# Kernel tuning notes

Measured on AMD Instinct MI355X. Metric: run time of the kernel, lower is better.

Reference implementation:

```python
import jax, jax.numpy as jnp
import numpy as np

WINDOW_SIZE = 11
CHANNEL = 1
SIGMA = 1.5


def _gaussian_window(window_size=WINDOW_SIZE, channel=CHANNEL, sigma=SIGMA):
    x = np.arange(window_size)
    g = np.exp(-((x - window_size // 2) ** 2) / (2.0 * sigma ** 2))
    g = g / g.sum()
    w2d = np.outer(g, g).astype(np.float32)  # [K,K]
    # depthwise conv kernel: [C_out=channel, C_in/groups=1, K, K]
    return jnp.asarray(np.broadcast_to(w2d, (channel, 1, window_size, window_size)))


def _dwconv(x, window):
    pad = WINDOW_SIZE // 2
    return jax.lax.conv_general_dilated(
        x, window,
        window_strides=(1, 1),
        padding=[(pad, pad), (pad, pad)],
        dimension_numbers=('NCHW', 'OIHW', 'NCHW'),
        feature_group_count=CHANNEL)


def _ssim(img1, img2, window):
    C1 = 0.01 ** 2
    C2 = 0.03 ** 2
    mu1 = _dwconv(img1, window)
    mu2 = _dwconv(img2, window)
    mu1_sq = mu1 * mu1
    mu2_sq = mu2 * mu2
    mu1_mu2 = mu1 * mu2
    sigma1_sq = _dwconv(img1 * img1, window) - mu1_sq
    sigma2_sq = _dwconv(img2 * img2, window) - mu2_sq
    sigma12 = _dwconv(img1 * img2, window) - mu1_mu2
    ssim_map = ((2.0 * mu1_mu2 + C1) * (2.0 * sigma12 + C2)) / (
        (mu1_sq + mu2_sq + C1) * (sigma1_sq + sigma2_sq + C2))
    return ssim_map.mean()


def setup_inputs() -> dict:
    key = jax.random.key(0)
    k1, k2 = jax.random.split(key)
    B, C, H, W = 64, 1, 512, 512
    pred = jax.random.uniform(k1, (B, C, H, W), dtype=jnp.float32)
    target = jax.random.uniform(k2, (B, C, H, W), dtype=jnp.float32)
    return {"pred": pred, "target": target}


def reference(pred, target):
    window = _gaussian_window()
    return 1.0 - _ssim(pred[:, :1], target[:, :1], window)
```

## Files before the change

kernel.cpp:

```cpp
#include <hip/hip_runtime.h>

#define BATCH 64
#define HH 512
#define WW 512
#define TH 32
#define KS 11
#define PADK 5
#define NPIX (64.0 * 512.0 * 512.0)
#define LROW (WW + 2 * PADK)

__global__ void __launch_bounds__(WW) ssim_main_kernel(
    const float* __restrict__ img1, const float* __restrict__ img2,
    double* __restrict__ accum) {
  constexpr float G[KS] = {
      0.00102838f, 0.00759884f, 0.03600087f, 0.10936069f, 0.21300553f,
      0.26601172f, 0.21300553f, 0.10936069f, 0.03600087f, 0.00759884f,
      0.00102838f};

  const int c  = threadIdx.x;
  const int r0 = blockIdx.x * TH;
  const int b  = blockIdx.y;

  const float* __restrict__ p1 = img1 + (size_t)b * (HH * WW);
  const float* __restrict__ p2 = img2 + (size_t)b * (HH * WW);

  __shared__ float2 sh[2][LROW];
  if (c < PADK) {
#pragma unroll
    for (int bi = 0; bi < 2; ++bi) {
      sh[bi][c] = make_float2(0.f, 0.f);
      sh[bi][WW + PADK + c] = make_float2(0.f, 0.f);
    }
  }

  float r1[KS], r2[KS], r11[KS], r22[KS], r12[KS];
#pragma unroll
  for (int k = 0; k < KS; ++k) { r1[k]=0.f; r2[k]=0.f; r11[k]=0.f; r22[k]=0.f; r12[k]=0.f; }

  float local = 0.f;

  float pa = 0.f, pb = 0.f;
  {
    const int rr = r0 - PADK;
    if (rr >= 0) {
      const int off = rr * WW + c;
      pa = p1[off];
      pb = p2[off];
    }
  }

  for (int ii = 0; ii < 4; ++ii) {
#pragma unroll
    for (int p = 0; p < KS; ++p) {
      const int i = ii * KS + p;
      const int buf = i & 1;

      const float ca = pa, cb = pb;
      {
        const int rn = r0 - PADK + i + 1;
        pa = 0.f; pb = 0.f;
        if (rn >= 0 && rn < HH) {
          const int off = rn * WW + c;
          pa = p1[off];
          pb = p2[off];
        }
      }

      sh[buf][PADK + c] = make_float2(ca, cb);
      __syncthreads();

      float h1 = 0.f, h2 = 0.f, h11 = 0.f, h22 = 0.f, h12 = 0.f;
#pragma unroll
      for (int k = 0; k < KS; ++k) {
        const float2 v = sh[buf][c + k];
        const float w  = G[k];
        const float aw = v.x * w;
        const float bw = v.y * w;
        h1  += aw;
        h2  += bw;
        h11 = fmaf(aw, v.x, h11);
        h22 = fmaf(bw, v.y, h22);
        h12 = fmaf(aw, v.y, h12);
      }

      r1[p] = h1; r2[p] = h2; r11[p] = h11; r22[p] = h22; r12[p] = h12;

      if (i >= 2 * PADK && i < TH + 2 * PADK) {
        float mu1 = 0.f, mu2 = 0.f, m11 = 0.f, m22 = 0.f, m12 = 0.f;
#pragma unroll
        for (int t = 0; t < KS; ++t) {
          const int s = (p + 1 + t) % KS;
          const float w = G[t];
          mu1 = fmaf(w, r1[s], mu1);
          mu2 = fmaf(w, r2[s], mu2);
          m11 = fmaf(w, r11[s], m11);
          m22 = fmaf(w, r22[s], m22);
          m12 = fmaf(w, r12[s], m12);
        }
        const float mu1s = mu1 * mu1;
        const float mu2s = mu2 * mu2;
        const float mu12 = mu1 * mu2;
        const float s11 = m11 - mu1s;
        const float s22 = m22 - mu2s;
        const float s12 = m12 - mu12;
        const float C1 = 1e-4f, C2 = 9e-4f;
        const float num = fmaf(2.f, mu12, C1) * fmaf(2.f, s12, C2);
        const float den = (mu1s + mu2s + C1) * (s11 + s22 + C2);
        local = fmaf(num, __builtin_amdgcn_rcpf(den), local);
      }
    }
  }

#pragma unroll
  for (int off = 32; off > 0; off >>= 1) local += __shfl_down(local, off, 64);

  __shared__ float wsum[WW / 64];
  const int wave = threadIdx.x >> 6;
  const int lane = threadIdx.x & 63;
  if (lane == 0) wsum[wave] = local;
  __syncthreads();
  if (threadIdx.x == 0) {
    float s = 0.f;
#pragma unroll
    for (int w = 0; w < WW / 64; ++w) s += wsum[w];
    atomicAdd(accum, (double)s);
  }
}

__global__ void ssim_final_kernel(const double* __restrict__ accum,
                                  float* __restrict__ out) {
  out[0] = 1.0f - (float)(accum[0] / NPIX);
}

extern "C" void kernel_launch(void* const* d_in, const int* in_sizes, int n_in,
                              void* d_out, int out_size, void* d_ws, size_t ws_size,
                              hipStream_t stream) {
  const float* img1 = (const float*)d_in[0];
  const float* img2 = (const float*)d_in[1];
  double* accum = (double*)d_ws;
  hipMemsetAsync(accum, 0, sizeof(double), stream);

  dim3 grid(HH / TH, BATCH);
  ssim_main_kernel<<<grid, WW, 0, stream>>>(img1, img2, accum);
  ssim_final_kernel<<<1, 1, 0, stream>>>(accum, (float*)d_out);
}
```

Measured before the change: 191.7 us.

## Precompute squared terms per pixel, merge sigma sums, batch four rows per sync

Each pixel now stores a float4 (a, b, a²+b², ab) in shared memory, so the horizontal pass runs four FMA chains instead of five and the vertical pass sums sigma1+sigma2 as a single field. Rows are staged four at a time, so there is one barrier per four rows instead of one per row. The outer loop is fully unrolled and launch bounds now request 4 blocks per SM. The trade-off is a larger shared-memory footprint and more register pressure, and the merged sum-of-squares term may lose a little floating-point accuracy.

```diff
diff --git a/kernel.cpp b/kernel.cpp
--- a/kernel.cpp
+++ b/kernel.cpp
@@ -6,10 +6,12 @@
 #define TH 32
 #define KS 11
 #define PADK 5
+#define RCH 4
+#define NCH 11
 #define NPIX (64.0 * 512.0 * 512.0)
 #define LROW (WW + 2 * PADK)
 
-__global__ void __launch_bounds__(WW) ssim_main_kernel(
+__global__ void __launch_bounds__(WW, 4) ssim_main_kernel(
     const float* __restrict__ img1, const float* __restrict__ img2,
     double* __restrict__ accum) {
   constexpr float G[KS] = {
@@ -24,88 +26,92 @@
   const float* __restrict__ p1 = img1 + (size_t)b * (HH * WW);
   const float* __restrict__ p2 = img2 + (size_t)b * (HH * WW);
 
-  __shared__ float2 sh[2][LROW];
+  __shared__ float4 s4[2][RCH][LROW];
   if (c < PADK) {
 #pragma unroll
-    for (int bi = 0; bi < 2; ++bi) {
-      sh[bi][c] = make_float2(0.f, 0.f);
-      sh[bi][WW + PADK + c] = make_float2(0.f, 0.f);
+    for (int bi = 0; bi < 2; ++bi)
+#pragma unroll
+      for (int r = 0; r < RCH; ++r) {
+        s4[bi][r][c]             = make_float4(0.f, 0.f, 0.f, 0.f);
+        s4[bi][r][WW + PADK + c] = make_float4(0.f, 0.f, 0.f, 0.f);
+      }
+  }
+
+  float rA[KS], rB[KS], rQ[KS], rP[KS];
+  float local = 0.f;
+
+  float pa[RCH], pb[RCH];
+#pragma unroll
+  for (int r = 0; r < RCH; ++r) {
+    const int rr = r0 - PADK + r;
+    pa[r] = 0.f; pb[r] = 0.f;
+    if (rr >= 0 && rr < HH) {
+      const int off = rr * WW + c;
+      pa[r] = p1[off];
+      pb[r] = p2[off];
     }
   }
 
-  float r1[KS], r2[KS], r11[KS], r22[KS], r12[KS];
 #pragma unroll
-  for (int k = 0; k < KS; ++k) { r1[k]=0.f; r2[k]=0.f; r11[k]=0.f; r22[k]=0.f; r12[k]=0.f; }
+  for (int ii = 0; ii < NCH; ++ii) {
+    const int buf = ii & 1;
 
-  float local = 0.f;
+#pragma unroll
+    for (int r = 0; r < RCH; ++r) {
+      const float a = pa[r], bb = pb[r];
+      s4[buf][r][PADK + c] = make_float4(a, bb, fmaf(a, a, bb * bb), a * bb);
+    }
+    __syncthreads();
 
-  float pa = 0.f, pb = 0.f;
-  {
-    const int rr = r0 - PADK;
-    if (rr >= 0) {
-      const int off = rr * WW + c;
-      pa = p1[off];
-      pb = p2[off];
-    }
-  }
-
-  for (int ii = 0; ii < 4; ++ii) {
+    if (ii + 1 < NCH) {
 #pragma unroll
-    for (int p = 0; p < KS; ++p) {
-      const int i = ii * KS + p;
-      const int buf = i & 1;
-
-      const float ca = pa, cb = pb;
-      {
-        const int rn = r0 - PADK + i + 1;
-        pa = 0.f; pb = 0.f;
-        if (rn >= 0 && rn < HH) {
-          const int off = rn * WW + c;
-          pa = p1[off];
-          pb = p2[off];
+      for (int r = 0; r < RCH; ++r) {
+        const int rr = r0 - PADK + (ii + 1) * RCH + r;
+        pa[r] = 0.f; pb[r] = 0.f;
+        if (rr >= 0 && rr < HH) {
+          const int off = rr * WW + c;
+          pa[r] = p1[off];
+          pb[r] = p2[off];
         }
       }
+    }
 
-      sh[buf][PADK + c] = make_float2(ca, cb);
-      __syncthreads();
+#pragma unroll
+    for (int p = 0; p < RCH; ++p) {
+      const int i = ii * RCH + p;
 
-      float h1 = 0.f, h2 = 0.f, h11 = 0.f, h22 = 0.f, h12 = 0.f;
+      float h1 = 0.f, h2 = 0.f, hq = 0.f, hp = 0.f;
 #pragma unroll
       for (int k = 0; k < KS; ++k) {
-        const float2 v = sh[buf][c + k];
+        const float4 v = s4[buf][p][c + k];
         const float w  = G[k];
-        const float aw = v.x * w;
-        const float bw = v.y * w;
-        h1  += aw;
-        h2  += bw;
-        h11 = fmaf(aw, v.x, h11);
-        h22 = fmaf(bw, v.y, h22);
-        h12 = fmaf(aw, v.y, h12);
+        h1 = fmaf(w, v.x, h1);
+        h2 = fmaf(w, v.y, h2);
+        hq = fmaf(w, v.z, hq);
+        hp = fmaf(w, v.w, hp);
       }
 
-      r1[p] = h1; r2[p] = h2; r11[p] = h11; r22[p] = h22; r12[p] = h12;
+      rA[i % KS] = h1; rB[i % KS] = h2; rQ[i % KS] = hq; rP[i % KS] = hp;
 
       if (i >= 2 * PADK && i < TH + 2 * PADK) {
-        float mu1 = 0.f, mu2 = 0.f, m11 = 0.f, m22 = 0.f, m12 = 0.f;
+        float mu1 = 0.f, mu2 = 0.f, mq = 0.f, mp = 0.f;
 #pragma unroll
         for (int t = 0; t < KS; ++t) {
-          const int s = (p + 1 + t) % KS;
+          const int s = (i + 1 + t) % KS;
           const float w = G[t];
-          mu1 = fmaf(w, r1[s], mu1);
-          mu2 = fmaf(w, r2[s], mu2);
-          m11 = fmaf(w, r11[s], m11);
-          m22 = fmaf(w, r22[s], m22);
-          m12 = fmaf(w, r12[s], m12);
+          mu1 = fmaf(w, rA[s], mu1);
+          mu2 = fmaf(w, rB[s], mu2);
+          mq  = fmaf(w, rQ[s], mq);
+          mp  = fmaf(w, rP[s], mp);
         }
         const float mu1s = mu1 * mu1;
         const float mu2s = mu2 * mu2;
         const float mu12 = mu1 * mu2;
-        const float s11 = m11 - mu1s;
-        const float s22 = m22 - mu2s;
-        const float s12 = m12 - mu12;
+        const float s12 = mp - mu12;
+        const float sqq = mq - mu1s - mu2s;
         const float C1 = 1e-4f, C2 = 9e-4f;
         const float num = fmaf(2.f, mu12, C1) * fmaf(2.f, s12, C2);
-        const float den = (mu1s + mu2s + C1) * (s11 + s22 + C2);
+        const float den = (mu1s + mu2s + C1) * (sqq + C2);
         local = fmaf(num, __builtin_amdgcn_rcpf(den), local);
       }
     }
```

New measurement: 184.3 us. 3.9% less time.

## Compute two columns per thread and merge squared sums into one blur

Applied to the files above, without the earlier changes.

Each thread now handles two adjacent columns, using float2 global loads and float4 shared reads, which reuses the overlapping 12-sample horizontal window. The a^2 and b^2 blurs are combined into a single a^2+b^2 blur, since SSIM only needs sigma1+sigma2. That cuts the separable-filter work from five quantities to four. Wasted iterations past the last needed row are skipped, and launch bounds are set to 256 threads with a minimum of 3 blocks. Register pressure rises with the doubled per-thread state, and the algebraic merge slightly changes float rounding.

```diff
diff --git a/kernel.cpp b/kernel.cpp
--- a/kernel.cpp
+++ b/kernel.cpp
@@ -8,8 +8,9 @@
 #define PADK 5
 #define NPIX (64.0 * 512.0 * 512.0)
 #define LROW (WW + 2 * PADK)
+#define NT 256
 
-__global__ void __launch_bounds__(WW) ssim_main_kernel(
+__global__ void __launch_bounds__(NT, 3) ssim_main_kernel(
     const float* __restrict__ img1, const float* __restrict__ img2,
     double* __restrict__ accum) {
   constexpr float G[KS] = {
@@ -17,7 +18,7 @@
       0.26601172f, 0.21300553f, 0.10936069f, 0.03600087f, 0.00759884f,
       0.00102838f};
 
-  const int c  = threadIdx.x;
+  const int t  = threadIdx.x;
   const int r0 = blockIdx.x * TH;
   const int b  = blockIdx.y;
 
@@ -25,27 +26,23 @@
   const float* __restrict__ p2 = img2 + (size_t)b * (HH * WW);
 
   __shared__ float2 sh[2][LROW];
-  if (c < PADK) {
+  if (t < PADK) {
 #pragma unroll
     for (int bi = 0; bi < 2; ++bi) {
-      sh[bi][c] = make_float2(0.f, 0.f);
-      sh[bi][WW + PADK + c] = make_float2(0.f, 0.f);
+      sh[bi][t]             = make_float2(0.f, 0.f);
+      sh[bi][WW + PADK + t] = make_float2(0.f, 0.f);
     }
   }
 
-  float r1[KS], r2[KS], r11[KS], r22[KS], r12[KS];
-#pragma unroll
-  for (int k = 0; k < KS; ++k) { r1[k]=0.f; r2[k]=0.f; r11[k]=0.f; r22[k]=0.f; r12[k]=0.f; }
+  float2 rA[KS], rB[KS], rQ[KS], rP[KS];
+  float lx = 0.f, ly = 0.f;
 
-  float local = 0.f;
-
-  float pa = 0.f, pb = 0.f;
+  float2 pa = make_float2(0.f, 0.f), pb = make_float2(0.f, 0.f);
   {
     const int rr = r0 - PADK;
     if (rr >= 0) {
-      const int off = rr * WW + c;
-      pa = p1[off];
-      pb = p2[off];
+      pa = ((const float2*)(p1 + (size_t)rr * WW))[t];
+      pb = ((const float2*)(p2 + (size_t)rr * WW))[t];
     }
   }
 
@@ -53,68 +50,92 @@
 #pragma unroll
     for (int p = 0; p < KS; ++p) {
       const int i = ii * KS + p;
-      const int buf = i & 1;
+      if (i < TH + 2 * PADK) {
+        const int buf = i & 1;
 
-      const float ca = pa, cb = pb;
-      {
-        const int rn = r0 - PADK + i + 1;
-        pa = 0.f; pb = 0.f;
-        if (rn >= 0 && rn < HH) {
-          const int off = rn * WW + c;
-          pa = p1[off];
-          pb = p2[off];
+        sh[buf][PADK + 2 * t]     = make_float2(pa.x, pb.x);
+        sh[buf][PADK + 2 * t + 1] = make_float2(pa.y, pb.y);
+
+        {
+          const int rn = r0 - PADK + i + 1;
+          pa = make_float2(0.f, 0.f);
+          pb = make_float2(0.f, 0.f);
+          if (rn >= 0 && rn < HH) {
+            pa = ((const float2*)(p1 + (size_t)rn * WW))[t];
+            pb = ((const float2*)(p2 + (size_t)rn * WW))[t];
+          }
         }
-      }
 
-      sh[buf][PADK + c] = make_float2(ca, cb);
-      __syncthreads();
+        __syncthreads();
 
-      float h1 = 0.f, h2 = 0.f, h11 = 0.f, h22 = 0.f, h12 = 0.f;
+        float av[12], bv[12];
+        const float4* sh4 = (const float4*)(&sh[buf][0]);
 #pragma unroll
-      for (int k = 0; k < KS; ++k) {
-        const float2 v = sh[buf][c + k];
-        const float w  = G[k];
-        const float aw = v.x * w;
-        const float bw = v.y * w;
-        h1  += aw;
-        h2  += bw;
-        h11 = fmaf(aw, v.x, h11);
-        h22 = fmaf(bw, v.y, h22);
-        h12 = fmaf(aw, v.y, h12);
-      }
+        for (int k = 0; k < 6; ++k) {
+          const float4 v = sh4[t + k];
+          av[2 * k]     = v.x;  bv[2 * k]     = v.y;
+          av[2 * k + 1] = v.z;  bv[2 * k + 1] = v.w;
+        }
 
-      r1[p] = h1; r2[p] = h2; r11[p] = h11; r22[p] = h22; r12[p] = h12;
+        float qv[12], pv[12];
+#pragma unroll
+        for (int j = 0; j < 12; ++j) {
+          qv[j] = fmaf(av[j], av[j], bv[j] * bv[j]);
+          pv[j] = av[j] * bv[j];
+        }
 
-      if (i >= 2 * PADK && i < TH + 2 * PADK) {
-        float mu1 = 0.f, mu2 = 0.f, m11 = 0.f, m22 = 0.f, m12 = 0.f;
+        float2 h1 = make_float2(0.f, 0.f), h2 = h1, hq = h1, hp = h1;
 #pragma unroll
-        for (int t = 0; t < KS; ++t) {
-          const int s = (p + 1 + t) % KS;
-          const float w = G[t];
-          mu1 = fmaf(w, r1[s], mu1);
-          mu2 = fmaf(w, r2[s], mu2);
-          m11 = fmaf(w, r11[s], m11);
-          m22 = fmaf(w, r22[s], m22);
-          m12 = fmaf(w, r12[s], m12);
+        for (int k = 0; k < KS; ++k) {
+          const float w = G[k];
+          h1.x = fmaf(w, av[k], h1.x);      h1.y = fmaf(w, av[k + 1], h1.y);
+          h2.x = fmaf(w, bv[k], h2.x);      h2.y = fmaf(w, bv[k + 1], h2.y);
+          hq.x = fmaf(w, qv[k], hq.x);      hq.y = fmaf(w, qv[k + 1], hq.y);
+          hp.x = fmaf(w, pv[k], hp.x);      hp.y = fmaf(w, pv[k + 1], hp.y);
         }
-        const float mu1s = mu1 * mu1;
-        const float mu2s = mu2 * mu2;
-        const float mu12 = mu1 * mu2;
-        const float s11 = m11 - mu1s;
-        const float s22 = m22 - mu2s;
-        const float s12 = m12 - mu12;
-        const float C1 = 1e-4f, C2 = 9e-4f;
-        const float num = fmaf(2.f, mu12, C1) * fmaf(2.f, s12, C2);
-        const float den = (mu1s + mu2s + C1) * (s11 + s22 + C2);
-        local = fmaf(num, __builtin_amdgcn_rcpf(den), local);
+        rA[p] = h1; rB[p] = h2; rQ[p] = hq; rP[p] = hp;
+
+        if (i >= 2 * PADK) {
+          float2 mu1 = make_float2(0.f, 0.f), mu2 = mu1, mq = mu1, mp = mu1;
+#pragma unroll
+          for (int tp = 0; tp < KS; ++tp) {
+            const int s = (p + 1 + tp) % KS;
+            const float w = G[tp];
+            mu1.x = fmaf(w, rA[s].x, mu1.x);  mu1.y = fmaf(w, rA[s].y, mu1.y);
+            mu2.x = fmaf(w, rB[s].x, mu2.x);  mu2.y = fmaf(w, rB[s].y, mu2.y);
+            mq.x  = fmaf(w, rQ[s].x, mq.x);   mq.y  = fmaf(w, rQ[s].y, mq.y);
+            mp.x  = fmaf(w, rP[s].x, mp.x);   mp.y  = fmaf(w, rP[s].y, mp.y);
+          }
+          const float C1 = 1e-4f, C2 = 9e-4f;
+          {
+            const float m1s = mu1.x * mu1.x, m2s = mu2.x * mu2.x;
+            const float m12 = mu1.x * mu2.x;
+            const float s12 = mp.x - m12;
+            const float sqq = mq.x - m1s - m2s;
+            const float num = fmaf(2.f, m12, C1) * fmaf(2.f, s12, C2);
+            const float den = (m1s + m2s + C1) * (sqq + C2);
+            lx = fmaf(num, __builtin_amdgcn_rcpf(den), lx);
+          }
+          {
+            const float m1s = mu1.y * mu1.y, m2s = mu2.y * mu2.y;
+            const float m12 = mu1.y * mu2.y;
+            const float s12 = mp.y - m12;
+            const float sqq = mq.y - m1s - m2s;
+            const float num = fmaf(2.f, m12, C1) * fmaf(2.f, s12, C2);
+            const float den = (m1s + m2s + C1) * (sqq + C2);
+            ly = fmaf(num, __builtin_amdgcn_rcpf(den), ly);
+          }
+        }
       }
     }
   }
 
+  float local = lx + ly;
+
 #pragma unroll
   for (int off = 32; off > 0; off >>= 1) local += __shfl_down(local, off, 64);
 
-  __shared__ float wsum[WW / 64];
+  __shared__ float wsum[NT / 64];
   const int wave = threadIdx.x >> 6;
   const int lane = threadIdx.x & 63;
   if (lane == 0) wsum[wave] = local;
@@ -122,7 +143,7 @@
   if (threadIdx.x == 0) {
     float s = 0.f;
 #pragma unroll
-    for (int w = 0; w < WW / 64; ++w) s += wsum[w];
+    for (int w = 0; w < NT / 64; ++w) s += wsum[w];
     atomicAdd(accum, (double)s);
   }
 }
@@ -141,6 +162,6 @@
   hipMemsetAsync(accum, 0, sizeof(double), stream);
 
   dim3 grid(HH / TH, BATCH);
-  ssim_main_kernel<<<grid, WW, 0, stream>>>(img1, img2, accum);
+  ssim_main_kernel<<<grid, NT, 0, stream>>>(img1, img2, accum);
   ssim_final_kernel<<<1, 1, 0, stream>>>(accum, (float*)d_out);
 }
```

Result: slower. 272.1 us (+42.0%).

## Process two rows per barrier, scatter vertical accumulation, fuse final reduction

Applied to the files above, without the earlier changes.

Each barrier step now stages two image rows in shared memory, which halves the number of __syncthreads calls. The vertical pass now scatters each horizontal result into a rotating accumulator ring instead of re-summing 11 stored rows, and it merges x²+y² into one channel, so four channels are filtered instead of five. The separate finalize kernel is removed: the last block, found through an atomic counter, writes the output. A waves_per_eu hint is also added. The risks are higher register pressure from the larger unrolled body and small numerical differences from the reordered sums.

```diff
diff --git a/kernel.cpp b/kernel.cpp
--- a/kernel.cpp
+++ b/kernel.cpp
@@ -6,12 +6,16 @@
 #define TH 32
 #define KS 11
 #define PADK 5
+#define LROW (WW + 2 * PADK)
+#define NT 512
+#define NBLK ((HH / TH) * BATCH)
 #define NPIX (64.0 * 512.0 * 512.0)
-#define LROW (WW + 2 * PADK)
 
-__global__ void __launch_bounds__(WW) ssim_main_kernel(
-    const float* __restrict__ img1, const float* __restrict__ img2,
-    double* __restrict__ accum) {
+__global__ void __launch_bounds__(NT)
+__attribute__((amdgpu_waves_per_eu(4)))
+ssim_main_kernel(const float* __restrict__ img1, const float* __restrict__ img2,
+                 double* __restrict__ accum, unsigned int* __restrict__ counter,
+                 float* __restrict__ out) {
   constexpr float G[KS] = {
       0.00102838f, 0.00759884f, 0.03600087f, 0.10936069f, 0.21300553f,
       0.26601172f, 0.21300553f, 0.10936069f, 0.03600087f, 0.00759884f,
@@ -24,89 +28,95 @@
   const float* __restrict__ p1 = img1 + (size_t)b * (HH * WW);
   const float* __restrict__ p2 = img2 + (size_t)b * (HH * WW);
 
-  __shared__ float2 sh[2][LROW];
+  __shared__ float2 sh[2][2][LROW];
   if (c < PADK) {
 #pragma unroll
-    for (int bi = 0; bi < 2; ++bi) {
-      sh[bi][c] = make_float2(0.f, 0.f);
-      sh[bi][WW + PADK + c] = make_float2(0.f, 0.f);
-    }
+    for (int bi = 0; bi < 2; ++bi)
+#pragma unroll
+      for (int r = 0; r < 2; ++r) {
+        sh[bi][r][c]             = make_float2(0.f, 0.f);
+        sh[bi][r][WW + PADK + c] = make_float2(0.f, 0.f);
+      }
   }
 
-  float r1[KS], r2[KS], r11[KS], r22[KS], r12[KS];
-#pragma unroll
-  for (int k = 0; k < KS; ++k) { r1[k]=0.f; r2[k]=0.f; r11[k]=0.f; r22[k]=0.f; r12[k]=0.f; }
-
+  float aA[KS], aB[KS], aQ[KS], aP[KS];
   float local = 0.f;
 
-  float pa = 0.f, pb = 0.f;
+  float pa0, pb0, pa1, pb1;
   {
-    const int rr = r0 - PADK;
-    if (rr >= 0) {
-      const int off = rr * WW + c;
-      pa = p1[off];
-      pb = p2[off];
-    }
+    const int rr0 = r0 - PADK;
+    const int rr1 = rr0 + 1;
+    pa0 = (rr0 >= 0) ? p1[rr0 * WW + c] : 0.f;
+    pb0 = (rr0 >= 0) ? p2[rr0 * WW + c] : 0.f;
+    pa1 = (rr1 >= 0) ? p1[rr1 * WW + c] : 0.f;
+    pb1 = (rr1 >= 0) ? p2[rr1 * WW + c] : 0.f;
   }
 
-  for (int ii = 0; ii < 4; ++ii) {
+  for (int g = 0; g < 2; ++g) {
+    const int ibase = 22 * g;
+    float2 (*bufE)[LROW] = sh[g & 1];
+    float2 (*bufO)[LROW] = sh[1 - (g & 1)];
 #pragma unroll
-    for (int p = 0; p < KS; ++p) {
-      const int i = ii * KS + p;
-      const int buf = i & 1;
+    for (int k = 0; k < KS; ++k) {
+      float2 (*B)[LROW] = (k & 1) ? bufO : bufE;
 
-      const float ca = pa, cb = pb;
+      B[0][PADK + c] = make_float2(pa0, pb0);
+      B[1][PADK + c] = make_float2(pa1, pb1);
+      __syncthreads();
+
       {
-        const int rn = r0 - PADK + i + 1;
-        pa = 0.f; pb = 0.f;
-        if (rn >= 0 && rn < HH) {
-          const int off = rn * WW + c;
-          pa = p1[off];
-          pb = p2[off];
-        }
+        const int rr  = r0 - PADK + ibase + 2 * k + 2;
+        const int rr1 = rr + 1;
+        const bool v0 = (rr  >= 0) && (rr  < HH);
+        const bool v1 = (rr1 >= 0) && (rr1 < HH);
+        pa0 = v0 ? p1[rr  * WW + c] : 0.f;
+        pb0 = v0 ? p2[rr  * WW + c] : 0.f;
+        pa1 = v1 ? p1[rr1 * WW + c] : 0.f;
+        pb1 = v1 ? p2[rr1 * WW + c] : 0.f;
       }
 
-      sh[buf][PADK + c] = make_float2(ca, cb);
-      __syncthreads();
+      if (ibase + 2 * k < TH + 2 * PADK) {
+#pragma unroll
+        for (int r = 0; r < 2; ++r) {
+          float h1 = 0.f, h2 = 0.f, hq = 0.f, hp = 0.f;
+#pragma unroll
+          for (int k2 = 0; k2 < KS; ++k2) {
+            const float2 v = B[r][c + k2];
+            const float q  = fmaf(v.x, v.x, v.y * v.y);
+            const float pp = v.x * v.y;
+            h1 = fmaf(G[k2], v.x, h1);
+            h2 = fmaf(G[k2], v.y, h2);
+            hq = fmaf(G[k2], q,   hq);
+            hp = fmaf(G[k2], pp,  hp);
+          }
 
-      float h1 = 0.f, h2 = 0.f, h11 = 0.f, h22 = 0.f, h12 = 0.f;
+          const int s0 = (2 * k + r) % KS;
+          aA[s0] = G[0] * h1; aB[s0] = G[0] * h2;
+          aQ[s0] = G[0] * hq; aP[s0] = G[0] * hp;
+
 #pragma unroll
-      for (int k = 0; k < KS; ++k) {
-        const float2 v = sh[buf][c + k];
-        const float w  = G[k];
-        const float aw = v.x * w;
-        const float bw = v.y * w;
-        h1  += aw;
-        h2  += bw;
-        h11 = fmaf(aw, v.x, h11);
-        h22 = fmaf(bw, v.y, h22);
-        h12 = fmaf(aw, v.y, h12);
-      }
+          for (int t = 1; t < KS; ++t) {
+            const int s = (2 * k + r - t + 22) % KS;
+            aA[s] = fmaf(G[t], h1, aA[s]);
+            aB[s] = fmaf(G[t], h2, aB[s]);
+            aQ[s] = fmaf(G[t], hq, aQ[s]);
+            aP[s] = fmaf(G[t], hp, aP[s]);
+          }
 
-      r1[p] = h1; r2[p] = h2; r11[p] = h11; r22[p] = h22; r12[p] = h12;
-
-      if (i >= 2 * PADK && i < TH + 2 * PADK) {
-        float mu1 = 0.f, mu2 = 0.f, m11 = 0.f, m22 = 0.f, m12 = 0.f;
-#pragma unroll
-        for (int t = 0; t < KS; ++t) {
-          const int s = (p + 1 + t) % KS;
-          const float w = G[t];
-          mu1 = fmaf(w, r1[s], mu1);
-          mu2 = fmaf(w, r2[s], mu2);
-          m11 = fmaf(w, r11[s], m11);
-          m22 = fmaf(w, r22[s], m22);
-          m12 = fmaf(w, r12[s], m12);
+          const int i = ibase + 2 * k + r;
+          if (i >= 2 * PADK && i < TH + 2 * PADK) {
+            const int s = (2 * k + r + 1) % KS;
+            const float mu1 = aA[s], mu2 = aB[s];
+            const float m1s = mu1 * mu1, m2s = mu2 * mu2, m12 = mu1 * mu2;
+            const float t12 = m1s + m2s;
+            const float s12 = aP[s] - m12;
+            const float sqq = aQ[s] - t12;
+            const float C1 = 1e-4f, C2 = 9e-4f;
+            const float num = fmaf(2.f, m12, C1) * fmaf(2.f, s12, C2);
+            const float den = (t12 + C1) * (sqq + C2);
+            local = fmaf(num, __builtin_amdgcn_rcpf(den), local);
+          }
         }
-        const float mu1s = mu1 * mu1;
-        const float mu2s = mu2 * mu2;
-        const float mu12 = mu1 * mu2;
-        const float s11 = m11 - mu1s;
-        const float s22 = m22 - mu2s;
-        const float s12 = m12 - mu12;
-        const float C1 = 1e-4f, C2 = 9e-4f;
-        const float num = fmaf(2.f, mu12, C1) * fmaf(2.f, s12, C2);
-        const float den = (mu1s + mu2s + C1) * (s11 + s22 + C2);
-        local = fmaf(num, __builtin_amdgcn_rcpf(den), local);
       }
     }
   }
@@ -114,7 +124,7 @@
 #pragma unroll
   for (int off = 32; off > 0; off >>= 1) local += __shfl_down(local, off, 64);
 
-  __shared__ float wsum[WW / 64];
+  __shared__ float wsum[NT / 64];
   const int wave = threadIdx.x >> 6;
   const int lane = threadIdx.x & 63;
   if (lane == 0) wsum[wave] = local;
@@ -122,14 +132,16 @@
   if (threadIdx.x == 0) {
     float s = 0.f;
 #pragma unroll
-    for (int w = 0; w < WW / 64; ++w) s += wsum[w];
+    for (int w = 0; w < NT / 64; ++w) s += wsum[w];
     atomicAdd(accum, (double)s);
+    __threadfence();
+    const unsigned int n = atomicAdd(counter, 1u);
+    if (n == NBLK - 1) {
+      __threadfence();
+      const double tot = atomicAdd(accum, 0.0);
+      out[0] = 1.0f - (float)(tot / NPIX);
+    }
   }
-}
-
-__global__ void ssim_final_kernel(const double* __restrict__ accum,
-                                  float* __restrict__ out) {
-  out[0] = 1.0f - (float)(accum[0] / NPIX);
 }
 
 extern "C" void kernel_launch(void* const* d_in, const int* in_sizes, int n_in,
@@ -138,9 +150,10 @@
   const float* img1 = (const float*)d_in[0];
   const float* img2 = (const float*)d_in[1];
   double* accum = (double*)d_ws;
-  hipMemsetAsync(accum, 0, sizeof(double), stream);
+  unsigned int* counter = (unsigned int*)((char*)d_ws + sizeof(double));
+  hipMemsetAsync(d_ws, 0, 16, stream);
 
   dim3 grid(HH / TH, BATCH);
-  ssim_main_kernel<<<grid, WW, 0, stream>>>(img1, img2, accum);
-  ssim_final_kernel<<<1, 1, 0, stream>>>(accum, (float*)d_out);
+  ssim_main_kernel<<<grid, NT, 0, stream>>>(img1, img2, accum, counter,
+                                            (float*)d_out);
 }
```

Measured after the change: 437.9 us. 2.28x slower.
